# Optimization experiments

Hardware: AMD Instinct MI355X
Metric: run time of the kernel (lower is better)

The kernel has to match this reference:

```python
import jax, jax.numpy as jnp
import numpy as np

N_X, N_NEIGH, D_IN, D_HID, D_OUT = 8192, 8192, 512, 32, 256
NEG_BIG = -9.0e15


def setup_inputs() -> dict:
    key = jax.random.key(0)
    ks = jax.random.split(key, 16)
    s_in = 1.0 / np.sqrt(D_IN)
    s_hid = 1.0 / np.sqrt(D_HID)
    return {
        "x": jax.random.normal(ks[0], (N_X, D_IN), jnp.float32),
        "neigh": jax.random.normal(ks[1], (N_NEIGH, D_IN), jnp.float32),
        "adj": jax.random.randint(ks[2], (N_X, N_NEIGH), 0, 2, jnp.int32),
        # att_x MLP: Linear(D_IN,D_HID) -> tanh -> Linear(D_HID,D_HID)
        "Wx1": jax.random.uniform(ks[3], (D_IN, D_HID), jnp.float32, -s_in, s_in),
        "bx1": jnp.zeros((D_HID,), jnp.float32),
        "Wx2": jax.random.uniform(ks[4], (D_HID, D_HID), jnp.float32, -s_hid, s_hid),
        "bx2": jnp.zeros((D_HID,), jnp.float32),
        # att_neigh MLP
        "Wn1": jax.random.uniform(ks[5], (D_IN, D_HID), jnp.float32, -s_in, s_in),
        "bn1": jnp.zeros((D_HID,), jnp.float32),
        "Wn2": jax.random.uniform(ks[6], (D_HID, D_HID), jnp.float32, -s_hid, s_hid),
        "bn2": jnp.zeros((D_HID,), jnp.float32),
        # fc_value, fc_x
        "Wv": jax.random.uniform(ks[7], (D_IN, D_OUT), jnp.float32, -s_in, s_in),
        "bv": jnp.zeros((D_OUT,), jnp.float32),
        "Wfx": jax.random.uniform(ks[8], (D_IN, D_OUT), jnp.float32, -s_in, s_in),
        "bfx": jnp.zeros((D_OUT,), jnp.float32),
    }


def reference(x, neigh, adj, Wx1, bx1, Wx2, bx2, Wn1, bn1, Wn2, bn2, Wv, bv, Wfx, bfx):
    # eval mode: dropouts are identity. edge_emb gather in original is dead code.
    neib_att = jnp.tanh(neigh @ Wn1 + bn1) @ Wn2 + bn2      # (N_neigh, H)
    value = neigh @ Wv + bv                                  # (N_neigh, D_OUT)
    x_att = jnp.tanh(x @ Wx1 + bx1) @ Wx2 + bx2              # (N_x, H)
    ws = jnp.einsum("nh,mh->nm", x_att, neib_att)            # (N_x, N_neigh)
    ws = jax.nn.leaky_relu(ws, negative_slope=0.01)
    ws = jnp.where(adj > 0, ws, jnp.float32(NEG_BIG))
    ws = jax.nn.softmax(ws, axis=1)
    agg_neib = ws @ value                                    # (N_x, D_OUT)
    out = jnp.concatenate([x @ Wfx + bfx, agg_neib], axis=1)  # (N_x, 2*D_OUT)
    return out
```

## Files before the change

### kernel.cpp

```cpp
#include <hip/hip_runtime.h>
#include <hip/hip_bf16.h>

#define NX 8192
#define NN 8192
#define DIN 512
#define DHID 32
#define DOUT 256

typedef __bf16 bf16x8 __attribute__((ext_vector_type(8)));
typedef float f32x4 __attribute__((ext_vector_type(4)));
typedef unsigned short u16x8 __attribute__((ext_vector_type(8)));

__device__ __forceinline__ unsigned short f2bf(float f) {
  __hip_bfloat16 h = __float2bfloat16(f);
  return __builtin_bit_cast(unsigned short, h);
}
__device__ __forceinline__ float bf2f(unsigned short u) {
  unsigned int v = ((unsigned int)u) << 16;
  return __builtin_bit_cast(float, v);
}
__device__ __forceinline__ f32x4 mfma16(u16x8 a, u16x8 b, f32x4 c) {
  return __builtin_amdgcn_mfma_f32_16x16x32_bf16(
      __builtin_bit_cast(bf16x8, a), __builtin_bit_cast(bf16x8, b), c, 0, 0, 0);
}
__device__ __forceinline__ u16x8 cvt8(float4 a0, float4 a1) {
  u16x8 u;
  u[0] = f2bf(a0.x); u[1] = f2bf(a0.y); u[2] = f2bf(a0.z); u[3] = f2bf(a0.w);
  u[4] = f2bf(a1.x); u[5] = f2bf(a1.y); u[6] = f2bf(a1.z); u[7] = f2bf(a1.w);
  return u;
}

__global__ __launch_bounds__(256) void k_wt(
    const float* __restrict__ Wv, const float* __restrict__ Wfx,
    const float* __restrict__ Wx1, const float* __restrict__ Wn1,
    const float* __restrict__ Wx2, const float* __restrict__ Wn2,
    unsigned short* __restrict__ WvT, unsigned short* __restrict__ WfxT,
    unsigned short* __restrict__ Wx1T, unsigned short* __restrict__ Wn1T,
    unsigned short* __restrict__ Wx2T, unsigned short* __restrict__ Wn2T) {
  const float* src; unsigned short* dst; int K, C;
  switch (blockIdx.y) {
    case 0:  src = Wv;  dst = WvT;  K = DIN; C = 256; break;
    case 1:  src = Wfx; dst = WfxT; K = DIN; C = 256; break;
    case 2:  src = Wx1; dst = Wx1T; K = DIN; C = 32;  break;
    case 3:  src = Wn1; dst = Wn1T; K = DIN; C = 32;  break;
    case 4:  src = Wx2; dst = Wx2T; K = 32;  C = 32;  break;
    default: src = Wn2; dst = Wn2T; K = 32;  C = 32;  break;
  }
  int tc = C >> 5, tk = K >> 5;
  if ((int)blockIdx.x >= tc * tk) return;
  int ik = blockIdx.x / tc, ic = blockIdx.x % tc;
  __shared__ float tile[32][33];
  int t = threadIdx.x, tx = t & 31, ty0 = t >> 5;
  #pragma unroll
  for (int q = 0; q < 4; ++q) {
    int ty = ty0 + q * 8;
    tile[ty][tx] = src[(ik * 32 + ty) * C + ic * 32 + tx];
  }
  __syncthreads();
  #pragma unroll
  for (int q = 0; q < 4; ++q) {
    int ty = ty0 + q * 8;
    dst[(ic * 32 + ty) * K + ik * 32 + tx] = f2bf(tile[tx][ty]);
  }
}

__global__ __launch_bounds__(256) void k_prep(
    const float* __restrict__ x, const float* __restrict__ neigh,
    const float* __restrict__ bfx, const float* __restrict__ bv,
    const float* __restrict__ bx1, const float* __restrict__ bn1,
    const unsigned short* __restrict__ WfxT, const unsigned short* __restrict__ WvT,
    const unsigned short* __restrict__ Wx1T, const unsigned short* __restrict__ Wn1T,
    float* __restrict__ out, unsigned short* __restrict__ Vp,
    unsigned short* __restrict__ Hx, unsigned short* __restrict__ Hn) {
  int job = blockIdx.y;
  const float* A = job ? neigh : x;
  const float* bias = job ? bv : bfx;
  const float* b1 = job ? bn1 : bx1;
  const unsigned short* WT = job ? WvT : WfxT;
  const unsigned short* W1T = job ? Wn1T : Wx1T;
  unsigned short* H = job ? Hn : Hx;
  __shared__ __align__(16) char As[2][64 * 64];
  int t = threadIdx.x;
  int lane = t & 63, w = t >> 6;
  int r = lane & 15, h4 = lane >> 4;
  int bm = blockIdx.x * 64;
  f32x4 acc[4][4];
  f32x4 acch[4];
  #pragma unroll
  for (int i = 0; i < 4; ++i) {
    acch[i] = (f32x4){0.f, 0.f, 0.f, 0.f};
    #pragma unroll
    for (int j = 0; j < 4; ++j) acc[i][j] = (f32x4){0.f, 0.f, 0.f, 0.f};
  }
  int srow = t >> 2, kq = t & 3;
  const float* ap = A + (long)(bm + srow) * DIN + kq * 8;
  float4 a0 = *reinterpret_cast<const float4*>(ap);
  float4 a1 = *reinterpret_cast<const float4*>(ap + 4);
  u16x8 pbc[4], pbhc;
  #pragma unroll
  for (int nt = 0; nt < 4; ++nt)
    pbc[nt] = *reinterpret_cast<const u16x8*>(WT + (w * 64 + nt * 16 + r) * DIN + h4 * 8);
  if (w < 2)
    pbhc = *reinterpret_cast<const u16x8*>(W1T + (w * 16 + r) * DIN + h4 * 8);
  int boff = (srow * 64 + kq * 16) ^ ((srow & 3) << 4);
  int buf = 0;
  for (int kk = 0; kk < 16; ++kk) {
    u16x8 u = cvt8(a0, a1);
    *reinterpret_cast<u16x8*>(&As[buf][0] + boff) = u;
    __syncthreads();
    u16x8 pbn[4], pbhn;
    if (kk < 15) {
      a0 = *reinterpret_cast<const float4*>(ap + (kk + 1) * 32);
      a1 = *reinterpret_cast<const float4*>(ap + (kk + 1) * 32 + 4);
      #pragma unroll
      for (int nt = 0; nt < 4; ++nt)
        pbn[nt] = *reinterpret_cast<const u16x8*>(
            WT + (w * 64 + nt * 16 + r) * DIN + (kk + 1) * 32 + h4 * 8);
      if (w < 2)
        pbhn = *reinterpret_cast<const u16x8*>(
            W1T + (w * 16 + r) * DIN + (kk + 1) * 32 + h4 * 8);
    }
    #pragma unroll
    for (int mt = 0; mt < 4; ++mt) {
      int ro = mt * 16 + r;
      int aoff = (ro * 64 + h4 * 16) ^ ((ro & 3) << 4);
      u16x8 pa = *reinterpret_cast<const u16x8*>(&As[buf][0] + aoff);
      #pragma unroll
      for (int nt = 0; nt < 4; ++nt) acc[mt][nt] = mfma16(pa, pbc[nt], acc[mt][nt]);
      if (w < 2) acch[mt] = mfma16(pa, pbhc, acch[mt]);
    }
    #pragma unroll
    for (int nt = 0; nt < 4; ++nt) pbc[nt] = pbn[nt];
    pbhc = pbhn;
    buf ^= 1;
  }
  #pragma unroll
  for (int mt = 0; mt < 4; ++mt)
    #pragma unroll
    for (int nt = 0; nt < 4; ++nt) {
      int c = w * 64 + nt * 16 + r;
      #pragma unroll
      for (int j = 0; j < 4; ++j) {
        int row = bm + mt * 16 + h4 * 4 + j;
        float v = acc[mt][nt][j] + bias[c];
        if (job == 0) out[(long)row * 512 + c] = v;
        else Vp[((row >> 3) * 256 + c) * 8 + (row & 7)] = f2bf(v);
      }
    }
  if (w < 2) {
    int c = w * 16 + r;
    float bb = b1[c];
    #pragma unroll
    for (int mt = 0; mt < 4; ++mt)
      #pragma unroll
      for (int j = 0; j < 4; ++j) {
        int row = bm + mt * 16 + h4 * 4 + j;
        H[row * DHID + c] = f2bf(tanhf(acch[mt][j] + bb));
      }
  }
}

__global__ __launch_bounds__(256) void k_att(
    const unsigned short* __restrict__ Hx, const unsigned short* __restrict__ Hn,
    const float* __restrict__ bx2, const float* __restrict__ bn2,
    const unsigned short* __restrict__ Wx2T, const unsigned short* __restrict__ Wn2T,
    unsigned short* __restrict__ xatt, unsigned short* __restrict__ natt) {
  const unsigned short* H; const float* b2; const unsigned short* WT; unsigned short* att;
  if (blockIdx.y == 0) { H = Hx; b2 = bx2; WT = Wx2T; att = xatt; }
  else                 { H = Hn; b2 = bn2; WT = Wn2T; att = natt; }
  int lane = threadIdx.x & 63, w = threadIdx.x >> 6;
  int r = lane & 15, h4 = lane >> 4;
  int row = blockIdx.x * 64 + w * 16 + r;
  u16x8 af = *reinterpret_cast<const u16x8*>(H + row * DHID + h4 * 8);
  u16x8 b0 = *reinterpret_cast<const u16x8*>(WT + r * DHID + h4 * 8);
  u16x8 b1 = *reinterpret_cast<const u16x8*>(WT + (16 + r) * DHID + h4 * 8);
  f32x4 z = {0.f, 0.f, 0.f, 0.f};
  f32x4 acc0 = mfma16(af, b0, z);
  f32x4 acc1 = mfma16(af, b1, z);
  int orow = blockIdx.x * 64 + w * 16 + h4 * 4;
  #pragma unroll
  for (int j = 0; j < 4; ++j) {
    att[(orow + j) * DHID + r]      = f2bf(acc0[j] + b2[r]);
    att[(orow + j) * DHID + 16 + r] = f2bf(acc1[j] + b2[16 + r]);
  }
}

__global__ __launch_bounds__(256, 4) void k_flash(
    const int* __restrict__ adj, const unsigned short* __restrict__ xatt,
    const unsigned short* __restrict__ natt, const unsigned short* __restrict__ Vp,
    float* __restrict__ out, unsigned short* __restrict__ accP,
    float* __restrict__ lP, int nc) {
  __shared__ unsigned short P[2][32 * 72];
  __shared__ float lpart[4][32];
  int t = threadIdx.x;
  int lane = t & 63, w = t >> 6;
  int r = lane & 15, h4 = lane >> 4;
  int rb = blockIdx.x * 32;
  int L = NN / nc;
  int base = blockIdx.y * L;
  int NIT = L / 64;
  u16x8 qf0 = *reinterpret_cast<const u16x8*>(xatt + (rb + r) * DHID + h4 * 8);
  u16x8 qf1 = *reinterpret_cast<const u16x8*>(xatt + (rb + 16 + r) * DHID + h4 * 8);
  f32x4 o[2][4];
  #pragma unroll
  for (int i = 0; i < 2; ++i)
    #pragma unroll
    for (int j = 0; j < 4; ++j) o[i][j] = (f32x4){0.f, 0.f, 0.f, 0.f};
  float psum[8];
  #pragma unroll
  for (int i = 0; i < 8; ++i) psum[i] = 0.f;
  int acur[8];
  #pragma unroll
  for (int rt = 0; rt < 2; ++rt)
    #pragma unroll
    for (int j = 0; j < 4; ++j)
      acur[rt * 4 + j] = adj[(long)(rb + rt * 16 + h4 * 4 + j) * NN + base + w * 16 + r];
  u16x8 kfc = *reinterpret_cast<const u16x8*>(natt + (base + w * 16 + r) * DHID + h4 * 8);
  int buf = 0;
  for (int it = 0; it < NIT; ++it) {
    int n0 = base + it * 64;
    int nn0 = (it + 1 < NIT) ? (n0 + 64) : n0;
    int anext[8];
    #pragma unroll
    for (int rt = 0; rt < 2; ++rt)
      #pragma unroll
      for (int j = 0; j < 4; ++j)
        anext[rt * 4 + j] = adj[(long)(rb + rt * 16 + h4 * 4 + j) * NN + nn0 + w * 16 + r];
    u16x8 kfn = *reinterpret_cast<const u16x8*>(natt + (nn0 + w * 16 + r) * DHID + h4 * 8);
    f32x4 z = {0.f, 0.f, 0.f, 0.f};
    f32x4 s0 = mfma16(qf0, kfc, z);
    f32x4 s1 = mfma16(qf1, kfc, z);
    unsigned short* Pb = &P[buf][0];
    #pragma unroll
    for (int rt = 0; rt < 2; ++rt) {
      f32x4 s = rt ? s1 : s0;
      #pragma unroll
      for (int j = 0; j < 4; ++j) {
        float sv = s[j];
        float lr = fminf(fmaxf(sv, 0.01f * sv), 60.f);
        float p = (acur[rt * 4 + j] > 0) ? __expf(lr) : 0.f;
        psum[rt * 4 + j] += p;
        Pb[(rt * 16 + h4 * 4 + j) * 72 + w * 16 + r] = f2bf(p);
      }
    }
    __syncthreads();
    #pragma unroll
    for (int kb = 0; kb < 2; ++kb) {
      u16x8 pa0 = *reinterpret_cast<const u16x8*>(Pb + r * 72 + kb * 32 + h4 * 8);
      u16x8 pa1 = *reinterpret_cast<const u16x8*>(Pb + (16 + r) * 72 + kb * 32 + h4 * 8);
      long vbase = ((long)((n0 + kb * 32) >> 3) + h4) * (DOUT * 8);
      #pragma unroll
      for (int nt = 0; nt < 4; ++nt) {
        u16x8 vf = *reinterpret_cast<const u16x8*>(Vp + vbase + (w * 64 + nt * 16 + r) * 8);
        o[0][nt] = mfma16(pa0, vf, o[0][nt]);
        o[1][nt] = mfma16(pa1, vf, o[1][nt]);
      }
    }
    #pragma unroll
    for (int q = 0; q < 8; ++q) acur[q] = anext[q];
    kfc = kfn;
    buf ^= 1;
  }
  #pragma unroll
  for (int q = 1; q < 16; q <<= 1)
    #pragma unroll
    for (int i = 0; i < 8; ++i) psum[i] += __shfl_xor(psum[i], q);
  if (r == 0) {
    #pragma unroll
    for (int rt = 0; rt < 2; ++rt)
      #pragma unroll
      for (int j = 0; j < 4; ++j)
        lpart[w][rt * 16 + h4 * 4 + j] = psum[rt * 4 + j];
  }
  __syncthreads();
  if (nc == 1) {
    #pragma unroll
    for (int rt = 0; rt < 2; ++rt)
      #pragma unroll
      for (int nt = 0; nt < 4; ++nt) {
        int c = w * 64 + nt * 16 + r;
        #pragma unroll
        for (int j = 0; j < 4; ++j) {
          int rl = rt * 16 + h4 * 4 + j;
          float l = lpart[0][rl] + lpart[1][rl] + lpart[2][rl] + lpart[3][rl];
          out[(long)(rb + rl) * 512 + 256 + c] = o[rt][nt][j] / l;
        }
      }
  } else {
    long cb = (long)blockIdx.y * NX;
    #pragma unroll
    for (int rt = 0; rt < 2; ++rt)
      #pragma unroll
      for (int nt = 0; nt < 4; ++nt) {
        int c = w * 64 + nt * 16 + r;
        #pragma unroll
        for (int j = 0; j < 4; ++j) {
          int rl = rt * 16 + h4 * 4 + j;
          accP[(cb + rb + rl) * DOUT + c] = f2bf(o[rt][nt][j]);
        }
      }
    if (t < 32)
      lP[blockIdx.y * NX + rb + t] =
          lpart[0][t] + lpart[1][t] + lpart[2][t] + lpart[3][t];
  }
}

__global__ __launch_bounds__(256) void k_combine(
    const unsigned short* __restrict__ accP, const float* __restrict__ lP,
    float* __restrict__ out, int nc) {
  long idx = (long)blockIdx.x * 256 + threadIdx.x;
  int row = (int)(idx >> 8), c = (int)(idx & 255);
  float s = 0.f, l = 0.f;
  for (int q = 0; q < nc; ++q) {
    s += bf2f(accP[(long)q * NX * DOUT + idx]);
    l += lP[q * NX + row];
  }
  out[(long)row * 512 + 256 + c] = s / l;
}

extern "C" void kernel_launch(void* const* d_in, const int* in_sizes, int n_in,
                              void* d_out, int out_size, void* d_ws, size_t ws_size,
                              hipStream_t stream) {
  const float* x    = (const float*)d_in[0];
  const float* neigh= (const float*)d_in[1];
  const int*   adj  = (const int*)d_in[2];
  const float* Wx1  = (const float*)d_in[3];
  const float* bx1  = (const float*)d_in[4];
  const float* Wx2  = (const float*)d_in[5];
  const float* bx2  = (const float*)d_in[6];
  const float* Wn1  = (const float*)d_in[7];
  const float* bn1  = (const float*)d_in[8];
  const float* Wn2  = (const float*)d_in[9];
  const float* bn2  = (const float*)d_in[10];
  const float* Wv   = (const float*)d_in[11];
  const float* bv   = (const float*)d_in[12];
  const float* Wfx  = (const float*)d_in[13];
  const float* bfx  = (const float*)d_in[14];
  float* out = (float*)d_out;
  char* ws = (char*)d_ws;

  unsigned short* xatt = (unsigned short*)(ws + 0);
  unsigned short* natt = (unsigned short*)(ws + 524288);
  unsigned short* Hx   = (unsigned short*)(ws + 1048576);
  unsigned short* Hn   = (unsigned short*)(ws + 1572864);
  unsigned short* Vp   = (unsigned short*)(ws + 2097152);
  unsigned short* WvT  = (unsigned short*)(ws + 6291456);
  unsigned short* WfxT = (unsigned short*)(ws + 6553600);
  unsigned short* Wx1T = (unsigned short*)(ws + 6815744);
  unsigned short* Wn1T = (unsigned short*)(ws + 6848512);
  unsigned short* Wx2T = (unsigned short*)(ws + 6881280);
  unsigned short* Wn2T = (unsigned short*)(ws + 6883328);

  const size_t OFF_ACC = 7340032;
  const size_t CHUNK_ACC = (size_t)NX * DOUT * 2;
  size_t need4 = OFF_ACC + 4 * (CHUNK_ACC + (size_t)NX * 4);
  size_t need2 = OFF_ACC + 2 * (CHUNK_ACC + (size_t)NX * 4);
  int nc = (ws_size >= need4) ? 4 : (ws_size >= need2) ? 2 : 1;
  unsigned short* accP = (unsigned short*)(ws + OFF_ACC);
  float* lP = (float*)(ws + OFF_ACC + (size_t)nc * CHUNK_ACC);

  k_wt<<<dim3(128, 6), 256, 0, stream>>>(Wv, Wfx, Wx1, Wn1, Wx2, Wn2,
                                         WvT, WfxT, Wx1T, Wn1T, Wx2T, Wn2T);
  k_prep<<<dim3(128, 2), 256, 0, stream>>>(x, neigh, bfx, bv, bx1, bn1,
                                           WfxT, WvT, Wx1T, Wn1T, out, Vp, Hx, Hn);
  k_att<<<dim3(128, 2), 256, 0, stream>>>(Hx, Hn, bx2, bn2, Wx2T, Wn2T, xatt, natt);
  k_flash<<<dim3(256, nc), 256, 0, stream>>>(adj, xatt, natt, Vp, out, accP, lP, nc);
  if (nc > 1)
    k_combine<<<dim3(NX * DOUT / 256), 256, 0, stream>>>(accP, lP, out, nc);
}
```

Baseline: 520.9 us.

## Enlarge flash tile to 128 rows with LDS-staged, double-buffered V chunks

```diff
diff --git a/kernel.cpp b/kernel.cpp
--- a/kernel.cpp
+++ b/kernel.cpp
@@ -185,123 +185,120 @@
   }
 }
 
-__global__ __launch_bounds__(256, 4) void k_flash(
+__global__ __launch_bounds__(1024, 2) void k_flash(
     const int* __restrict__ adj, const unsigned short* __restrict__ xatt,
     const unsigned short* __restrict__ natt, const unsigned short* __restrict__ Vp,
     float* __restrict__ out, unsigned short* __restrict__ accP,
     float* __restrict__ lP, int nc) {
-  __shared__ unsigned short P[2][32 * 72];
-  __shared__ float lpart[4][32];
+  __shared__ unsigned short P[2][128 * 40];
+  __shared__ __align__(16) unsigned short Vl[2][4 * 256 * 8];
+  __shared__ float lpart[16][16];
   int t = threadIdx.x;
   int lane = t & 63, w = t >> 6;
   int r = lane & 15, h4 = lane >> 4;
-  int rb = blockIdx.x * 32;
+  int rt = w >> 1, ns = w & 1;
+  int fid = blockIdx.y * gridDim.x + blockIdx.x;
+  int g = 8 / nc;
+  int m8 = fid & 7;
+  int my = m8 / g;
+  int mx = (fid >> 3) * g + (m8 % g);
+  int rb = mx * 128;
   int L = NN / nc;
-  int base = blockIdx.y * L;
-  int NIT = L / 64;
-  u16x8 qf0 = *reinterpret_cast<const u16x8*>(xatt + (rb + r) * DHID + h4 * 8);
-  u16x8 qf1 = *reinterpret_cast<const u16x8*>(xatt + (rb + 16 + r) * DHID + h4 * 8);
-  f32x4 o[2][4];
-  #pragma unroll
-  for (int i = 0; i < 2; ++i)
-    #pragma unroll
-    for (int j = 0; j < 4; ++j) o[i][j] = (f32x4){0.f, 0.f, 0.f, 0.f};
-  float psum[8];
-  #pragma unroll
-  for (int i = 0; i < 8; ++i) psum[i] = 0.f;
-  int acur[8];
-  #pragma unroll
-  for (int rt = 0; rt < 2; ++rt)
+  int base = my * L;
+  int NIT = L / 32;
+  int lastn = base + L - 32;
+  u16x8 qf = *reinterpret_cast<const u16x8*>(xatt + (rb + rt * 16 + r) * DHID + h4 * 8);
+  f32x4 o[8];
+  #pragma unroll
+  for (int i = 0; i < 8; ++i) o[i] = (f32x4){0.f, 0.f, 0.f, 0.f};
+  float psum[4] = {0.f, 0.f, 0.f, 0.f};
+  int adjA[4], adjB[4];
+  u16x8 kfA, kfB;
+  #pragma unroll
+  for (int j = 0; j < 4; ++j) {
+    long ro = (long)(rb + rt * 16 + h4 * 4 + j) * NN + ns * 16 + r;
+    adjA[j] = __builtin_nontemporal_load(&adj[ro + base]);
+    adjB[j] = __builtin_nontemporal_load(&adj[ro + base + 32]);
+  }
+  kfA = *reinterpret_cast<const u16x8*>(natt + (base + ns * 16 + r) * DHID + h4 * 8);
+  kfB = *reinterpret_cast<const u16x8*>(natt + (base + 32 + ns * 16 + r) * DHID + h4 * 8);
+  {
+    u16x8 v0 = *reinterpret_cast<const u16x8*>(Vp + (long)base * 256 + t * 8);
+    *reinterpret_cast<u16x8*>(&Vl[0][0] + t * 8) = v0;
+  }
+  u16x8 vregA = *reinterpret_cast<const u16x8*>(Vp + (long)(base + 32) * 256 + t * 8);
+  __syncthreads();
+  int pb = 0, vb = 0;
+  for (int it = 0; it < NIT; ++it) {
+    int n0 = base + it * 32;
+    f32x4 z = {0.f, 0.f, 0.f, 0.f};
+    f32x4 s = mfma16(qf, kfA, z);
+    unsigned short* Pb = &P[pb][0];
+    #pragma unroll
+    for (int j = 0; j < 4; ++j) {
+      float sv = s[j];
+      float lr = fminf(fmaxf(sv, 0.01f * sv), 60.f);
+      float p = (adjA[j] > 0) ? __expf(lr) : 0.f;
+      psum[j] += p;
+      Pb[(rt * 16 + h4 * 4 + j) * 40 + ns * 16 + r] = f2bf(p);
+    }
+    __syncthreads();
+    #pragma unroll
+    for (int j = 0; j < 4; ++j) adjA[j] = adjB[j];
+    kfA = kfB;
+    int nn = n0 + 64 <= lastn ? n0 + 64 : lastn;
     #pragma unroll
     for (int j = 0; j < 4; ++j)
-      acur[rt * 4 + j] = adj[(long)(rb + rt * 16 + h4 * 4 + j) * NN + base + w * 16 + r];
-  u16x8 kfc = *reinterpret_cast<const u16x8*>(natt + (base + w * 16 + r) * DHID + h4 * 8);
-  int buf = 0;
-  for (int it = 0; it < NIT; ++it) {
-    int n0 = base + it * 64;
-    int nn0 = (it + 1 < NIT) ? (n0 + 64) : n0;
-    int anext[8];
-    #pragma unroll
-    for (int rt = 0; rt < 2; ++rt)
-      #pragma unroll
-      for (int j = 0; j < 4; ++j)
-        anext[rt * 4 + j] = adj[(long)(rb + rt * 16 + h4 * 4 + j) * NN + nn0 + w * 16 + r];
-    u16x8 kfn = *reinterpret_cast<const u16x8*>(natt + (nn0 + w * 16 + r) * DHID + h4 * 8);
-    f32x4 z = {0.f, 0.f, 0.f, 0.f};
-    f32x4 s0 = mfma16(qf0, kfc, z);
-    f32x4 s1 = mfma16(qf1, kfc, z);
-    unsigned short* Pb = &P[buf][0];
-    #pragma unroll
-    for (int rt = 0; rt < 2; ++rt) {
-      f32x4 s = rt ? s1 : s0;
+      adjB[j] = __builtin_nontemporal_load(
+          &adj[(long)(rb + rt * 16 + h4 * 4 + j) * NN + nn + ns * 16 + r]);
+    kfB = *reinterpret_cast<const u16x8*>(natt + (nn + ns * 16 + r) * DHID + h4 * 8);
+    u16x8 vregB = *reinterpret_cast<const u16x8*>(Vp + (long)nn * 256 + t * 8);
+    u16x8 pa = *reinterpret_cast<const u16x8*>(&P[pb][0] + (rt * 16 + r) * 40 + h4 * 8);
+    #pragma unroll
+    for (int ct = 0; ct < 8; ++ct) {
+      u16x8 vf = *reinterpret_cast<const u16x8*>(
+          &Vl[vb][0] + (h4 * 256 + ns * 128 + ct * 16 + r) * 8);
+      o[ct] = mfma16(pa, vf, o[ct]);
+    }
+    *reinterpret_cast<u16x8*>(&Vl[vb ^ 1][0] + t * 8) = vregA;
+    vregA = vregB;
+    pb ^= 1; vb ^= 1;
+  }
+  #pragma unroll
+  for (int q = 1; q < 16; q <<= 1)
+    #pragma unroll
+    for (int j = 0; j < 4; ++j) psum[j] += __shfl_xor(psum[j], q);
+  if (r == 0) {
+    #pragma unroll
+    for (int j = 0; j < 4; ++j) lpart[w][h4 * 4 + j] = psum[j];
+  }
+  __syncthreads();
+  int cb = ns * 128;
+  if (nc == 1) {
+    #pragma unroll
+    for (int ct = 0; ct < 8; ++ct) {
+      int c = cb + ct * 16 + r;
       #pragma unroll
       for (int j = 0; j < 4; ++j) {
-        float sv = s[j];
-        float lr = fminf(fmaxf(sv, 0.01f * sv), 60.f);
-        float p = (acur[rt * 4 + j] > 0) ? __expf(lr) : 0.f;
-        psum[rt * 4 + j] += p;
-        Pb[(rt * 16 + h4 * 4 + j) * 72 + w * 16 + r] = f2bf(p);
+        int rl = rt * 16 + h4 * 4 + j;
+        float l = lpart[2 * rt][h4 * 4 + j] + lpart[2 * rt + 1][h4 * 4 + j];
+        out[(long)(rb + rl) * 512 + 256 + c] = o[ct][j] / l;
       }
     }
-    __syncthreads();
-    #pragma unroll
-    for (int kb = 0; kb < 2; ++kb) {
-      u16x8 pa0 = *reinterpret_cast<const u16x8*>(Pb + r * 72 + kb * 32 + h4 * 8);
-      u16x8 pa1 = *reinterpret_cast<const u16x8*>(Pb + (16 + r) * 72 + kb * 32 + h4 * 8);
-      long vbase = ((long)((n0 + kb * 32) >> 3) + h4) * (DOUT * 8);
-      #pragma unroll
-      for (int nt = 0; nt < 4; ++nt) {
-        u16x8 vf = *reinterpret_cast<const u16x8*>(Vp + vbase + (w * 64 + nt * 16 + r) * 8);
-        o[0][nt] = mfma16(pa0, vf, o[0][nt]);
-        o[1][nt] = mfma16(pa1, vf, o[1][nt]);
+  } else {
+    long cbase = (long)my * NX;
+    #pragma unroll
+    for (int ct = 0; ct < 8; ++ct) {
+      int c = cb + ct * 16 + r;
+      #pragma unroll
+      for (int j = 0; j < 4; ++j) {
+        int rl = rt * 16 + h4 * 4 + j;
+        accP[(cbase + rb + rl) * DOUT + c] = f2bf(o[ct][j]);
       }
     }
-    #pragma unroll
-    for (int q = 0; q < 8; ++q) acur[q] = anext[q];
-    kfc = kfn;
-    buf ^= 1;
-  }
-  #pragma unroll
-  for (int q = 1; q < 16; q <<= 1)
-    #pragma unroll
-    for (int i = 0; i < 8; ++i) psum[i] += __shfl_xor(psum[i], q);
-  if (r == 0) {
-    #pragma unroll
-    for (int rt = 0; rt < 2; ++rt)
-      #pragma unroll
-      for (int j = 0; j < 4; ++j)
-        lpart[w][rt * 16 + h4 * 4 + j] = psum[rt * 4 + j];
-  }
-  __syncthreads();
-  if (nc == 1) {
-    #pragma unroll
-    for (int rt = 0; rt < 2; ++rt)
-      #pragma unroll
-      for (int nt = 0; nt < 4; ++nt) {
-        int c = w * 64 + nt * 16 + r;
-        #pragma unroll
-        for (int j = 0; j < 4; ++j) {
-          int rl = rt * 16 + h4 * 4 + j;
-          float l = lpart[0][rl] + lpart[1][rl] + lpart[2][rl] + lpart[3][rl];
-          out[(long)(rb + rl) * 512 + 256 + c] = o[rt][nt][j] / l;
-        }
-      }
-  } else {
-    long cb = (long)blockIdx.y * NX;
-    #pragma unroll
-    for (int rt = 0; rt < 2; ++rt)
-      #pragma unroll
-      for (int nt = 0; nt < 4; ++nt) {
-        int c = w * 64 + nt * 16 + r;
-        #pragma unroll
-        for (int j = 0; j < 4; ++j) {
-          int rl = rt * 16 + h4 * 4 + j;
-          accP[(cb + rb + rl) * DOUT + c] = f2bf(o[rt][nt][j]);
-        }
-      }
-    if (t < 32)
-      lP[blockIdx.y * NX + rb + t] =
-          lpart[0][t] + lpart[1][t] + lpart[2][t] + lpart[3][t];
+    if (t < 128)
+      lP[my * NX + rb + t] =
+          lpart[2 * (t >> 4)][t & 15] + lpart[2 * (t >> 4) + 1][t & 15];
   }
 }
 
@@ -351,7 +348,7 @@
   unsigned short* Wx2T = (unsigned short*)(ws + 6881280);
   unsigned short* Wn2T = (unsigned short*)(ws + 6883328);
 
-  const size_t OFF_ACC = 7340032;
+  const size_t OFF_ACC = 16777216;
   const size_t CHUNK_ACC = (size_t)NX * DOUT * 2;
   size_t need4 = OFF_ACC + 4 * (CHUNK_ACC + (size_t)NX * 4);
   size_t need2 = OFF_ACC + 2 * (CHUNK_ACC + (size_t)NX * 4);
@@ -364,7 +361,7 @@
   k_prep<<<dim3(128, 2), 256, 0, stream>>>(x, neigh, bfx, bv, bx1, bn1,
                                            WfxT, WvT, Wx1T, Wn1T, out, Vp, Hx, Hn);
   k_att<<<dim3(128, 2), 256, 0, stream>>>(Hx, Hn, bx2, bn2, Wx2T, Wn2T, xatt, natt);
-  k_flash<<<dim3(256, nc), 256, 0, stream>>>(adj, xatt, natt, Vp, out, accP, lP, nc);
+  k_flash<<<dim3(64, nc), 1024, 0, stream>>>(adj, xatt, natt, Vp, out, accP, lP, nc);
   if (nc > 1)
     k_combine<<<dim3(NX * DOUT / 256), 256, 0, stream>>>(accP, lP, out, nc);
 }
```

After: 488.5 us. -6.2%, faster.
